# Kernel optimization log

Measured on AMD Instinct MI355X. Metric: run time of the kernel, lower is better.

The kernel has to match this reference:

```python
import jax, jax.numpy as jnp
import numpy as np

N_IN, N_OUT, N_POOL = 1_500_000, 400_000, 60_000
CIN, COUT, K = 4, 64, 27
BN_EPS = 1e-5


def setup_inputs() -> dict:
    key = jax.random.key(0)
    k1, k2, k3, k4 = jax.random.split(key, 4)
    x = jax.random.normal(k1, (N_IN, CIN), dtype=jnp.float32)
    weight = jax.random.normal(k2, (K, CIN, COUT), dtype=jnp.float32) * 0.1
    gamma = jnp.ones((COUT,), dtype=jnp.float32)
    beta = jnp.zeros((COUT,), dtype=jnp.float32)
    neigh_idx = jax.random.randint(k3, (N_OUT, K), 0, N_IN, dtype=jnp.int32)
    pool_idx = jax.random.randint(k4, (N_POOL, 8), 0, N_OUT, dtype=jnp.int32)
    return {"x": x, "weight": weight, "gamma": gamma, "beta": beta,
            "neigh_idx": neigh_idx, "pool_idx": pool_idx, "depth": 4}


def reference(x, weight, gamma, beta, neigh_idx, pool_idx, depth):
    # OctreeConv (stride 2, nempty): gather 27 neighbors per output node,
    # contract with [27, Cin, Cout] weight.
    gathered = x[neigh_idx]                       # [N_out, 27, Cin]
    y = jnp.einsum('nkc,kco->no', gathered, weight)  # [N_out, Cout]
    # BatchNorm1d (training mode: batch statistics over the node dim)
    mean = jnp.mean(y, axis=0)
    var = jnp.var(y, axis=0)
    y = (y - mean) * jax.lax.rsqrt(var + BN_EPS) * gamma + beta
    # ReLU
    y = jax.nn.relu(y)
    # OctreeMaxPool (nempty): max over 8 children per parent node
    pooled = jnp.max(y[pool_idx], axis=1)         # [N_pool, Cout]
    return pooled, depth - 2
```

## Files before the change

### kernel.cpp

```cpp
#include <hip/hip_runtime.h>

#define COUT 64
#define KNB 27
#define BN_EPS 1e-5f
#define NBANDS 6
#define NGRP 4

typedef __attribute__((ext_vector_type(8))) short short8v;
typedef __attribute__((ext_vector_type(4))) float f32x4;

union U4S8 { uint4 u; short8v s; };

static __device__ __forceinline__ unsigned f2bf(float f) {
    unsigned u = __float_as_uint(f);
    return (u + 0x7fffu + ((u >> 16) & 1u)) >> 16;
}

static __device__ __forceinline__ void glds4(const void* g, void* l) {
    __builtin_amdgcn_global_load_lds(
        (const __attribute__((address_space(1))) void*)g,
        (__attribute__((address_space(3))) void*)l, 4, 0, 0);
}

__global__ __launch_bounds__(256) void xconv_kernel(
    const float4* __restrict__ x, uint2* __restrict__ xb, int n_in)
{
    int i = blockIdx.x * 256 + threadIdx.x;
    if (i >= n_in) return;
    float4 r = x[i];
    uint2 o;
    o.x = f2bf(r.x) | (f2bf(r.y) << 16);
    o.y = f2bf(r.z) | (f2bf(r.w) << 16);
    xb[i] = o;
}

__global__ __launch_bounds__(256, 2) void conv_stats_kernel(
    const uint2* __restrict__ xb,
    const float* __restrict__ w,
    const int*   __restrict__ nidx,
    unsigned short* __restrict__ yb,
    float*       __restrict__ stats,
    int n_out, int band)
{
    const int lane = threadIdx.x & 63;
    const int wid  = threadIdx.x >> 6;
    const int row  = lane & 15;
    const int grp  = lane >> 4;
    const int gwave   = blockIdx.x * 4 + wid;
    const int nwaves  = gridDim.x * 4;
    const int ngroups = (n_out + 15) >> 4;
    const int npairs  = (ngroups + NGRP - 1) / NGRP;
    const int niter   = (npairs + nwaves - 1) / nwaves;

    __shared__ uint4 blds[16 * 64];
    __shared__ unsigned xls[4][NGRP * 16][64];

#pragma unroll
    for (int pp = 0; pp < 4; ++pp) {
        const int pair = wid * 4 + pp;
        const int kb = pair >> 2, t = pair & 3;
        const int o = t * 16 + row;
        unsigned e[8];
#pragma unroll
        for (int j = 0; j < 8; ++j) {
            const int k = kb * 32 + grp * 8 + j;
            float v = (k < KNB * 4) ? w[k * COUT + o] : 0.0f;
            e[j] = f2bf(v);
        }
        uint4 f;
        f.x = e[0] | (e[1] << 16);
        f.y = e[2] | (e[3] << 16);
        f.z = e[4] | (e[5] << 16);
        f.w = e[6] | (e[7] << 16);
        blds[pair * 64 + lane] = f;
    }
#pragma unroll
    for (int s = 0; s < NGRP * 16; ++s) xls[wid][s][lane] = 0u;
    __syncthreads();

    float sum[4]   = {0.f, 0.f, 0.f, 0.f};
    float sumsq[4] = {0.f, 0.f, 0.f, 0.f};

    auto load_ia = [&](int pp, int (&ia)[NGRP][4][2]) {
#pragma unroll
        for (int gi = 0; gi < NGRP; ++gi) {
            const int gg = pp * NGRP + gi;
            const int nodeg = (gg << 4) + row;
            const bool vn = (gg < ngroups) && (nodeg < n_out);
#pragma unroll
            for (int kb = 0; kb < 4; ++kb)
#pragma unroll
                for (int h = 0; h < 2; ++h) {
                    const int nb = kb * 8 + grp * 2 + h;
                    ia[gi][kb][h] = (vn && nb < KNB) ? nidx[nodeg * KNB + nb] : -1;
                }
        }
    };

    int ia_cur[NGRP][4][2];
    load_ia(gwave, ia_cur);

    for (int it = 0; it < niter; ++it) {
        const int p = gwave + it * nwaves;

        int ia_nxt[NGRP][4][2];

#pragma unroll
        for (int b = 0; b < NBANDS; ++b) {
            const int lo = b * band;
#pragma unroll
            for (int gi = 0; gi < NGRP; ++gi)
#pragma unroll
                for (int kb = 0; kb < 4; ++kb)
#pragma unroll
                    for (int h = 0; h < 2; ++h) {
                        const int idx = ia_cur[gi][kb][h];
                        if ((unsigned)(idx - lo) < (unsigned)band) {
                            const unsigned* src = (const unsigned*)&xb[idx];
                            const int s = gi * 16 + kb * 4 + h * 2;
                            glds4(src,     &xls[wid][s][0]);
                            glds4(src + 1, &xls[wid][s + 1][0]);
                        }
                    }
            if (b == 0) load_ia(p + nwaves, ia_nxt);
            __builtin_amdgcn_sched_barrier(0);
            if (b < NBANDS - 1) {
                asm volatile("s_waitcnt vmcnt(16)" ::: "memory");
            } else {
                asm volatile("s_waitcnt vmcnt(0)" ::: "memory");
            }
            __builtin_amdgcn_s_barrier();
            __builtin_amdgcn_sched_barrier(0);
        }

        if (p < npairs) {
#pragma unroll
            for (int gi = 0; gi < NGRP; ++gi) {
                f32x4 acc[4];
#pragma unroll
                for (int t = 0; t < 4; ++t) acc[t] = (f32x4){0.f, 0.f, 0.f, 0.f};
#pragma unroll
                for (int kb = 0; kb < 4; ++kb) {
                    const int s = gi * 16 + kb * 4;
                    U4S8 a;
                    a.u = make_uint4(xls[wid][s + 0][lane], xls[wid][s + 1][lane],
                                     xls[wid][s + 2][lane], xls[wid][s + 3][lane]);
#pragma unroll
                    for (int t = 0; t < 4; ++t) {
                        U4S8 bb;
                        bb.u = blds[(kb * 4 + t) * 64 + lane];
                        acc[t] = __builtin_amdgcn_mfma_f32_16x16x32_bf16(
                                     a.s, bb.s, acc[t], 0, 0, 0);
                    }
                }

                const int gbase = (p * NGRP + gi) << 4;
#pragma unroll
                for (int t = 0; t < 4; ++t) {
#pragma unroll
                    for (int j = 0; j < 4; ++j) {
                        const int nr = gbase + grp * 4 + j;
                        const float v = acc[t][j];
                        if (nr < n_out)
                            yb[(size_t)nr * COUT + t * 16 + row] =
                                (unsigned short)f2bf(v);
                        sum[t]   += v;
                        sumsq[t]  = fmaf(v, v, sumsq[t]);
                    }
                }
            }
        }

#pragma unroll
        for (int gi = 0; gi < NGRP; ++gi)
#pragma unroll
            for (int kb = 0; kb < 4; ++kb)
#pragma unroll
                for (int h = 0; h < 2; ++h)
                    ia_cur[gi][kb][h] = ia_nxt[gi][kb][h];
    }

    __syncthreads();
    float (*redS)[4][16] = (float (*)[4][16])&xls[0][0][0];
    float (*redQ)[4][16] = (float (*)[4][16])&xls[1][0][0];
#pragma unroll
    for (int t = 0; t < 4; ++t) {
        float s = sum[t], q = sumsq[t];
        s += __shfl_xor(s, 16); s += __shfl_xor(s, 32);
        q += __shfl_xor(q, 16); q += __shfl_xor(q, 32);
        if (lane < 16) { redS[wid][t][lane] = s; redQ[wid][t][lane] = q; }
    }
    __syncthreads();
    if (threadIdx.x < 128) {
        const int which = threadIdx.x >> 6;
        const int o = threadIdx.x & 63;
        const int t = o >> 4, c = o & 15;
        float tot;
        if (which == 0)
            tot = redS[0][t][c] + redS[1][t][c] + redS[2][t][c] + redS[3][t][c];
        else
            tot = redQ[0][t][c] + redQ[1][t][c] + redQ[2][t][c] + redQ[3][t][c];
        atomicAdd(&stats[which * COUT + o], tot);
    }
}

__global__ void finalize_kernel(
    const float* __restrict__ stats,
    const float* __restrict__ gamma,
    const float* __restrict__ beta,
    float*       __restrict__ scaleshift,
    const int*   __restrict__ depth,
    float*       __restrict__ out_tail,
    int n_out, int write_depth)
{
    int o = threadIdx.x;
    if (o < COUT) {
        float invn  = 1.0f / (float)n_out;
        float mean  = stats[o] * invn;
        float var   = stats[COUT + o] * invn - mean * mean;
        float scale = gamma[o] * rsqrtf(var + BN_EPS);
        scaleshift[o]        = scale;
        scaleshift[COUT + o] = beta[o] - mean * scale;
    }
    if (o == 0 && write_depth) {
        out_tail[0] = (float)(depth[0] - 2);
    }
}

__global__ __launch_bounds__(256) void pool_kernel(
    const uint2*  __restrict__ yb2,
    const int*    __restrict__ pidx,
    const float4* __restrict__ scaleshift4,
    float4*       __restrict__ out4,
    int n_pool)
{
    const int t = blockIdx.x * 256 + threadIdx.x;
    const int q = t & 15;
    const int n = t >> 4;
    if (n >= n_pool) return;

    const float4 sc = scaleshift4[q];
    const float4 sh = scaleshift4[16 + q];

    int idx[8];
#pragma unroll
    for (int j = 0; j < 8; ++j) idx[j] = pidx[n * 8 + j];

    uint2 v[8];
#pragma unroll
    for (int j = 0; j < 8; ++j) v[j] = yb2[(size_t)idx[j] * 16 + q];

    float4 m = make_float4(-INFINITY, -INFINITY, -INFINITY, -INFINITY);
#pragma unroll
    for (int j = 0; j < 8; ++j) {
        float f0 = __uint_as_float(v[j].x << 16);
        float f1 = __uint_as_float(v[j].x & 0xffff0000u);
        float f2 = __uint_as_float(v[j].y << 16);
        float f3 = __uint_as_float(v[j].y & 0xffff0000u);
        m.x = fmaxf(m.x, fmaf(f0, sc.x, sh.x));
        m.y = fmaxf(m.y, fmaf(f1, sc.y, sh.y));
        m.z = fmaxf(m.z, fmaf(f2, sc.z, sh.z));
        m.w = fmaxf(m.w, fmaf(f3, sc.w, sh.w));
    }
    m.x = fmaxf(m.x, 0.f); m.y = fmaxf(m.y, 0.f);
    m.z = fmaxf(m.z, 0.f); m.w = fmaxf(m.w, 0.f);
    out4[(size_t)n * 16 + q] = m;
}

extern "C" void kernel_launch(void* const* d_in, const int* in_sizes, int n_in_args,
                              void* d_out, int out_size, void* d_ws, size_t ws_size,
                              hipStream_t stream)
{
    const float4* x     = (const float4*)d_in[0];
    const float*  w     = (const float*) d_in[1];
    const float*  gamma = (const float*) d_in[2];
    const float*  beta  = (const float*) d_in[3];
    const int*    nidx  = (const int*)   d_in[4];
    const int*    pidx  = (const int*)   d_in[5];
    const int*    depth = (const int*)   d_in[6];

    const int n_in   = in_sizes[0] / 4;
    const int n_out  = in_sizes[4] / KNB;
    const int n_pool = in_sizes[5] / 8;
    const int band   = (n_in + NBANDS - 1) / NBANDS;

    float* stats      = (float*)d_ws;
    float* scaleshift = (float*)((char*)d_ws + 512);
    unsigned short* yb = (unsigned short*)((char*)d_ws + 1024);
    size_t yb_bytes   = ((size_t)n_out * COUT * 2 + 255) & ~(size_t)255;
    uint2* xb         = (uint2*)((char*)d_ws + 1024 + yb_bytes);
    float* out        = (float*)d_out;

    hipMemsetAsync(stats, 0, 2 * COUT * sizeof(float), stream);

    xconv_kernel<<<(n_in + 255) / 256, 256, 0, stream>>>(x, xb, n_in);

    conv_stats_kernel<<<512, 256, 0, stream>>>(xb, w, nidx, yb, stats,
                                               n_out, band);

    const int write_depth = (out_size > n_pool * COUT) ? 1 : 0;
    finalize_kernel<<<1, 64, 0, stream>>>(stats, gamma, beta, scaleshift,
                                          depth, out + (size_t)n_pool * COUT,
                                          n_out, write_depth);

    const int pool_blocks = (n_pool * 16 + 255) / 256;
    pool_kernel<<<pool_blocks, 256, 0, stream>>>((const uint2*)yb, pidx,
                                                 (const float4*)scaleshift,
                                                 (float4*)out, n_pool);
}
```

Baseline: 145.6 us.

## Keep weight fragments in registers, drop index prefetch, raise occupancy to 3 blocks/CU

Moves the bf16 weight B-fragments from shared memory into per-lane registers and removes the software prefetch of next-iteration neighbor indices. Node groups per wave drop from 4 to 3, so each block uses less LDS and fewer registers; launch bounds go to 3 blocks per CU and the grid to 768 blocks. The aim is more resident waves to hide the latency of the banded gather, at the cost of exposing the index loads at the start of each iteration. Stats accumulation now happens only for valid rows.

Result: slower. 156.4 us (+7.4%).

```diff
diff --git a/kernel.cpp b/kernel.cpp
--- a/kernel.cpp
+++ b/kernel.cpp
@@ -4,7 +4,7 @@
 #define KNB 27
 #define BN_EPS 1e-5f
 #define NBANDS 6
-#define NGRP 4
+#define NGRP 3
 
 typedef __attribute__((ext_vector_type(8))) short short8v;
 typedef __attribute__((ext_vector_type(4))) float f32x4;
@@ -34,7 +34,7 @@
     xb[i] = o;
 }
 
-__global__ __launch_bounds__(256, 2) void conv_stats_kernel(
+__global__ __launch_bounds__(256, 3) void conv_stats_kernel(
     const uint2* __restrict__ xb,
     const float* __restrict__ w,
     const int*   __restrict__ nidx,
@@ -52,28 +52,25 @@
     const int npairs  = (ngroups + NGRP - 1) / NGRP;
     const int niter   = (npairs + nwaves - 1) / nwaves;
 
-    __shared__ uint4 blds[16 * 64];
     __shared__ unsigned xls[4][NGRP * 16][64];
 
-#pragma unroll
-    for (int pp = 0; pp < 4; ++pp) {
-        const int pair = wid * 4 + pp;
-        const int kb = pair >> 2, t = pair & 3;
-        const int o = t * 16 + row;
-        unsigned e[8];
-#pragma unroll
-        for (int j = 0; j < 8; ++j) {
-            const int k = kb * 32 + grp * 8 + j;
-            float v = (k < KNB * 4) ? w[k * COUT + o] : 0.0f;
-            e[j] = f2bf(v);
-        }
-        uint4 f;
-        f.x = e[0] | (e[1] << 16);
-        f.y = e[2] | (e[3] << 16);
-        f.z = e[4] | (e[5] << 16);
-        f.w = e[6] | (e[7] << 16);
-        blds[pair * 64 + lane] = f;
-    }
+    U4S8 bfrag[4][4];
+#pragma unroll
+    for (int t = 0; t < 4; ++t)
+#pragma unroll
+        for (int kb = 0; kb < 4; ++kb) {
+            const int o = t * 16 + row;
+            unsigned e[8];
+#pragma unroll
+            for (int j = 0; j < 8; ++j) {
+                const int k = kb * 32 + grp * 8 + j;
+                float v = (k < KNB * 4) ? w[k * COUT + o] : 0.0f;
+                e[j] = f2bf(v);
+            }
+            bfrag[t][kb].u = make_uint4(e[0] | (e[1] << 16), e[2] | (e[3] << 16),
+                                        e[4] | (e[5] << 16), e[6] | (e[7] << 16));
+        }
+
 #pragma unroll
     for (int s = 0; s < NGRP * 16; ++s) xls[wid][s][lane] = 0u;
     __syncthreads();
@@ -81,12 +78,15 @@
     float sum[4]   = {0.f, 0.f, 0.f, 0.f};
     float sumsq[4] = {0.f, 0.f, 0.f, 0.f};
 
-    auto load_ia = [&](int pp, int (&ia)[NGRP][4][2]) {
+    for (int it = 0; it < niter; ++it) {
+        const int p = gwave + it * nwaves;
+
+        int ia[NGRP][4][2];
 #pragma unroll
         for (int gi = 0; gi < NGRP; ++gi) {
-            const int gg = pp * NGRP + gi;
+            const int gg = p * NGRP + gi;
             const int nodeg = (gg << 4) + row;
-            const bool vn = (gg < ngroups) && (nodeg < n_out);
+            const bool vn = (gg < ngroups);
 #pragma unroll
             for (int kb = 0; kb < 4; ++kb)
 #pragma unroll
@@ -95,15 +95,6 @@
                     ia[gi][kb][h] = (vn && nb < KNB) ? nidx[nodeg * KNB + nb] : -1;
                 }
         }
-    };
-
-    int ia_cur[NGRP][4][2];
-    load_ia(gwave, ia_cur);
-
-    for (int it = 0; it < niter; ++it) {
-        const int p = gwave + it * nwaves;
-
-        int ia_nxt[NGRP][4][2];
 
 #pragma unroll
         for (int b = 0; b < NBANDS; ++b) {
@@ -114,7 +105,7 @@
                 for (int kb = 0; kb < 4; ++kb)
 #pragma unroll
                     for (int h = 0; h < 2; ++h) {
-                        const int idx = ia_cur[gi][kb][h];
+                        const int idx = ia[gi][kb][h];
                         if ((unsigned)(idx - lo) < (unsigned)band) {
                             const unsigned* src = (const unsigned*)&xb[idx];
                             const int s = gi * 16 + kb * 4 + h * 2;
@@ -122,7 +113,6 @@
                             glds4(src + 1, &xls[wid][s + 1][0]);
                         }
                     }
-            if (b == 0) load_ia(p + nwaves, ia_nxt);
             __builtin_amdgcn_sched_barrier(0);
             if (b < NBANDS - 1) {
                 asm volatile("s_waitcnt vmcnt(16)" ::: "memory");
@@ -133,51 +123,41 @@
             __builtin_amdgcn_sched_barrier(0);
         }
 
-        if (p < npairs) {
-#pragma unroll
-            for (int gi = 0; gi < NGRP; ++gi) {
-                f32x4 acc[4];
-#pragma unroll
-                for (int t = 0; t < 4; ++t) acc[t] = (f32x4){0.f, 0.f, 0.f, 0.f};
-#pragma unroll
-                for (int kb = 0; kb < 4; ++kb) {
-                    const int s = gi * 16 + kb * 4;
-                    U4S8 a;
-                    a.u = make_uint4(xls[wid][s + 0][lane], xls[wid][s + 1][lane],
-                                     xls[wid][s + 2][lane], xls[wid][s + 3][lane]);
-#pragma unroll
-                    for (int t = 0; t < 4; ++t) {
-                        U4S8 bb;
-                        bb.u = blds[(kb * 4 + t) * 64 + lane];
-                        acc[t] = __builtin_amdgcn_mfma_f32_16x16x32_bf16(
-                                     a.s, bb.s, acc[t], 0, 0, 0);
-                    }
-                }
-
-                const int gbase = (p * NGRP + gi) << 4;
-#pragma unroll
-                for (int t = 0; t < 4; ++t) {
-#pragma unroll
-                    for (int j = 0; j < 4; ++j) {
-                        const int nr = gbase + grp * 4 + j;
-                        const float v = acc[t][j];
-                        if (nr < n_out)
-                            yb[(size_t)nr * COUT + t * 16 + row] =
-                                (unsigned short)f2bf(v);
+#pragma unroll
+        for (int gi = 0; gi < NGRP; ++gi) {
+            const int gg = p * NGRP + gi;
+            if (gg >= ngroups) continue;
+            f32x4 acc[4];
+#pragma unroll
+            for (int t = 0; t < 4; ++t) acc[t] = (f32x4){0.f, 0.f, 0.f, 0.f};
+#pragma unroll
+            for (int kb = 0; kb < 4; ++kb) {
+                const int s = gi * 16 + kb * 4;
+                U4S8 a;
+                a.u = make_uint4(xls[wid][s + 0][lane], xls[wid][s + 1][lane],
+                                 xls[wid][s + 2][lane], xls[wid][s + 3][lane]);
+#pragma unroll
+                for (int t = 0; t < 4; ++t)
+                    acc[t] = __builtin_amdgcn_mfma_f32_16x16x32_bf16(
+                                 a.s, bfrag[t][kb].s, acc[t], 0, 0, 0);
+            }
+
+            const int gbase = gg << 4;
+#pragma unroll
+            for (int t = 0; t < 4; ++t) {
+#pragma unroll
+                for (int j = 0; j < 4; ++j) {
+                    const int nr = gbase + grp * 4 + j;
+                    const float v = acc[t][j];
+                    if (nr < n_out) {
+                        yb[(size_t)nr * COUT + t * 16 + row] =
+                            (unsigned short)f2bf(v);
                         sum[t]   += v;
                         sumsq[t]  = fmaf(v, v, sumsq[t]);
                     }
                 }
             }
         }
-
-#pragma unroll
-        for (int gi = 0; gi < NGRP; ++gi)
-#pragma unroll
-            for (int kb = 0; kb < 4; ++kb)
-#pragma unroll
-                for (int h = 0; h < 2; ++h)
-                    ia_cur[gi][kb][h] = ia_nxt[gi][kb][h];
     }
 
     __syncthreads();
@@ -295,7 +275,7 @@
 
     xconv_kernel<<<(n_in + 255) / 256, 256, 0, stream>>>(x, xb, n_in);
 
-    conv_stats_kernel<<<512, 256, 0, stream>>>(xb, w, nidx, yb, stats,
+    conv_stats_kernel<<<768, 256, 0, stream>>>(xb, w, nidx, yb, stats,
                                                n_out, band);
 
     const int write_depth = (out_size > n_pool * COUT) ? 1 : 0;
```
